# Performance work log

Measured on AMD Instinct MI355X. Metric: run time of the kernel, lower is better.

Reference implementation:

```python
import jax, jax.numpy as jnp
import numpy as np

TOP_K = 2  # k experts per token


def setup_inputs() -> dict:
    key = jax.random.key(0)
    ks = jax.random.split(key, 6)
    B, L, D, E, F = 2, 2048, 1024, 8, 4096
    x = jax.random.normal(ks[0], (B, L, D), dtype=jnp.float32)
    Wg = jax.random.normal(ks[1], (D, E), dtype=jnp.float32) * (D ** -0.5)
    W1 = jax.random.normal(ks[2], (E, D, F), dtype=jnp.float32) * (D ** -0.5)
    b1 = jnp.zeros((E, F), dtype=jnp.float32)
    W2 = jax.random.normal(ks[3], (E, F, D), dtype=jnp.float32) * (F ** -0.5)
    b2 = jnp.zeros((E, D), dtype=jnp.float32)
    return {"x": x, "Wg": Wg, "W1": W1, "b1": b1, "W2": W2, "b2": b2}


def reference(x, Wg, W1, b1, W2, b2):
    b, l, d = x.shape
    E = Wg.shape[1]
    xt = x.reshape(b * l, d)                      # (N, D)
    N = xt.shape[0]
    # Router: sigmoid gate, top-k (gate weights are NOT renormalized in the source)
    S = jax.nn.sigmoid(xt @ Wg)                   # (N, E)
    G, I = jax.lax.top_k(S, TOP_K)                # (N, k) each
    # Dense equivalent of per-expert gather-MLP-scatter: run every expert
    # on every token, then combine with the sparse top-k routing weights.
    h = jax.nn.gelu(jnp.einsum('nd,edf->enf', xt, W1) + b1[:, None, :])  # (E, N, F)
    y = jnp.einsum('enf,efd->end', h, W2) + b2[:, None, :]               # (E, N, D)
    # combine[n, e] = sum of gate values for slots routed to expert e
    combine = jnp.zeros((N, E), dtype=x.dtype).at[jnp.arange(N)[:, None], I].add(G)
    out = jnp.einsum('ne,end->nd', combine, y)    # (N, D)
    return out.reshape(b, l, d)
```

## Files before the change

### kernel.cpp

```cpp
#include <hip/hip_runtime.h>
#include <math.h>

typedef __bf16 bf16_t;
typedef __attribute__((ext_vector_type(8))) __bf16 bf16x8;
typedef __attribute__((ext_vector_type(4))) __bf16 bf16x4;
typedef __attribute__((ext_vector_type(4))) float f32x4;

#define NTOK 4096
#define DDIM 1024
#define FDIM 4096
#define NEXP 8
#define CAP  4096
#define HROWS (2*NTOK + 128)
#define NPAIR (2*NTOK)

#define GLOAD_LDS16(g, l) \
  __builtin_amdgcn_global_load_lds((__attribute__((address_space(1))) void*)(g), \
                                   (__attribute__((address_space(3))) void*)(l), 16, 0, 0)

__device__ __forceinline__ float fast_gelu(float v) {
  float u = 0.7978845608028654f * (v + 0.044715f * v * v * v);
  float uc = fminf(fmaxf(u, -10.f), 10.f);
  float t = __builtin_amdgcn_exp2f(2.885390081777927f * uc);
  float th = (t - 1.f) * __builtin_amdgcn_rcpf(t + 1.f);
  return 0.5f * v * (1.0f + th);
}

__global__ __launch_bounds__(256) void init_kernel(const float4* __restrict__ x4,
                                                   bf16x4* __restrict__ xbf4,
                                                   int n4, int* __restrict__ cnts) {
  int i = blockIdx.x * 256 + threadIdx.x;
  if (i < n4) {
    float4 v = x4[i];
    bf16x4 o;
    o.x = (bf16_t)v.x; o.y = (bf16_t)v.y; o.z = (bf16_t)v.z; o.w = (bf16_t)v.w;
    xbf4[i] = o;
  }
  if (i < NEXP) cnts[i] = 0;
}

__global__ __launch_bounds__(256) void transpose_cvt(const float* __restrict__ in,
                                                     bf16_t* __restrict__ outp,
                                                     int R, int C) {
  __shared__ float tile[64][65];
  int e = blockIdx.z;
  const float* ip = in + (size_t)e * R * C;
  bf16_t* op = outp + (size_t)e * R * C;
  int c0 = blockIdx.x * 64, r0 = blockIdx.y * 64;
  int rr = threadIdx.x >> 4;
  int cc = (threadIdx.x & 15) * 4;
#pragma unroll
  for (int p = 0; p < 4; p++) {
    float4 v = *(const float4*)(ip + (size_t)(r0 + p * 16 + rr) * C + c0 + cc);
    tile[p * 16 + rr][cc + 0] = v.x;
    tile[p * 16 + rr][cc + 1] = v.y;
    tile[p * 16 + rr][cc + 2] = v.z;
    tile[p * 16 + rr][cc + 3] = v.w;
  }
  __syncthreads();
  int c = threadIdx.x >> 3;
  int r8 = (threadIdx.x & 7) * 8;
#pragma unroll
  for (int p = 0; p < 2; p++) {
    int cp = c + p * 32;
    bf16x8 o;
#pragma unroll
    for (int i = 0; i < 8; i++) o[i] = (bf16_t)tile[r8 + i][cp];
    *(bf16x8*)(op + (size_t)(c0 + cp) * R + r0 + r8) = o;
  }
}

__global__ __launch_bounds__(256) void router_kernel(const float* __restrict__ x,
                                                     const float* __restrict__ Wg,
                                                     int* __restrict__ tokL,
                                                     int* __restrict__ cnts,
                                                     int* __restrict__ pairE,
                                                     int* __restrict__ pairS,
                                                     float* __restrict__ pairG) {
  int wid = threadIdx.x >> 6, lane = threadIdx.x & 63;
  int n = blockIdx.x * 4 + wid;
  const float* xr = x + (size_t)n * DDIM;
  double acc[NEXP];
#pragma unroll
  for (int e = 0; e < NEXP; e++) acc[e] = 0.0;
  for (int i = 0; i < DDIM / 64; i++) {
    int d = i * 64 + lane;
    float xv = xr[d];
    const float* wr = Wg + (size_t)d * NEXP;
#pragma unroll
    for (int e = 0; e < NEXP; e++) acc[e] += (double)xv * (double)wr[e];
  }
#pragma unroll
  for (int e = 0; e < NEXP; e++) {
    double v = acc[e];
#pragma unroll
    for (int off = 32; off; off >>= 1) v += __shfl_xor(v, off);
    acc[e] = v;
  }
  if (lane == 0) {
    int i1 = -1, i2 = -1;
    double s1 = -1e300, s2 = -1e300;
#pragma unroll
    for (int e = 0; e < NEXP; e++) {
      double v = acc[e];
      if (v > s1) { s2 = s1; i2 = i1; s1 = v; i1 = e; }
      else if (v > s2) { s2 = v; i2 = e; }
    }
    float g1 = 1.0f / (1.0f + expf((float)(-s1)));
    float g2 = 1.0f / (1.0f + expf((float)(-s2)));
    int p1 = atomicAdd(&cnts[i1], 1);
    tokL[i1 * CAP + p1] = n;
    int p2 = atomicAdd(&cnts[i2], 1);
    tokL[i2 * CAP + p2] = n;
    pairE[2 * n] = i1; pairS[2 * n] = p1; pairG[2 * n] = g1;
    pairE[2 * n + 1] = i2; pairS[2 * n + 1] = p2; pairG[2 * n + 1] = g2;
  }
}

__global__ void offs_kernel(const int* __restrict__ cnts, int* __restrict__ offs) {
  if (threadIdx.x == 0) {
    int s = 0;
    for (int e = 0; e < NEXP; e++) { offs[e] = s; s += cnts[e]; }
    offs[NEXP] = s;
  }
}

__global__ __launch_bounds__(256) void gemm1_kernel(
    const bf16_t* __restrict__ xbf, const bf16_t* __restrict__ wt1,
    const float* __restrict__ b1, const int* __restrict__ tokL,
    const int* __restrict__ cnts, const int* __restrict__ offs,
    bf16_t* __restrict__ H) {
  const int e = blockIdx.z;
  const int cnt = cnts[e];
  const int m0 = blockIdx.y * 128;
  if (m0 >= cnt) return;
  const int n0 = blockIdx.x * 128;
  const int t = threadIdx.x;

  __shared__ alignas(16) bf16_t As[128 * 32];
  __shared__ alignas(16) bf16_t Bs[128 * 32];

  const int sr = t >> 2;
  const int sc = (t & 3) * 8;
  const int r0 = m0 + sr, r1 = m0 + sr + 64;
  const int tok0 = (r0 < cnt) ? tokL[e * CAP + r0] : 0;
  const int tok1 = (r1 < cnt) ? tokL[e * CAP + r1] : 0;
  const bf16_t* gA0 = xbf + (size_t)tok0 * DDIM + sc;
  const bf16_t* gA1 = xbf + (size_t)tok1 * DDIM + sc;
  const bf16_t* wte = wt1 + (size_t)e * FDIM * DDIM;
  const bf16_t* gB0 = wte + (size_t)(n0 + sr) * DDIM + sc;
  const bf16_t* gB1 = wte + (size_t)(n0 + sr + 64) * DDIM + sc;
  bf16_t* lA0 = As + t * 8; bf16_t* lA1 = As + 2048 + t * 8;
  bf16_t* lB0 = Bs + t * 8; bf16_t* lB1 = Bs + 2048 + t * 8;

  const int lane = t & 63, w = t >> 6;
  const int wm = (w >> 1) * 64, wn = (w & 1) * 64;
  const int lid = lane & 15, quad = lane >> 4;

  f32x4 acc[4][4] = {};
  for (int kk = 0; kk < DDIM; kk += 32) {
    GLOAD_LDS16(gA0 + kk, lA0);
    GLOAD_LDS16(gA1 + kk, lA1);
    GLOAD_LDS16(gB0 + kk, lB0);
    GLOAD_LDS16(gB1 + kk, lB1);
    __syncthreads();
    bf16x8 af[4], bfm[4];
#pragma unroll
    for (int i = 0; i < 4; i++)
      af[i] = *(const bf16x8*)(As + (wm + i * 16 + lid) * 32 + quad * 8);
#pragma unroll
    for (int j = 0; j < 4; j++)
      bfm[j] = *(const bf16x8*)(Bs + (wn + j * 16 + lid) * 32 + quad * 8);
#pragma unroll
    for (int i = 0; i < 4; i++)
#pragma unroll
      for (int j = 0; j < 4; j++)
        acc[i][j] = __builtin_amdgcn_mfma_f32_16x16x32_bf16(af[i], bfm[j], acc[i][j], 0, 0, 0);
    __syncthreads();
  }

  const float* b1e = b1 + (size_t)e * FDIM;
  const int offe = offs[e];
#pragma unroll
  for (int i = 0; i < 4; i++) {
#pragma unroll
    for (int reg = 0; reg < 4; reg++) {
      int pos = m0 + wm + i * 16 + quad * 4 + reg;
      if (pos >= cnt) continue;
      size_t hrow = (size_t)(offe + pos);
#pragma unroll
      for (int j = 0; j < 4; j++) {
        int col = n0 + wn + j * 16 + lid;
        float v = acc[i][j][reg] + b1e[col];
        H[hrow * FDIM + col] = (bf16_t)fast_gelu(v);
      }
    }
  }
}

__global__ __launch_bounds__(256) void gemm2_kernel(
    const bf16_t* __restrict__ H, const bf16_t* __restrict__ wt2,
    const int* __restrict__ cnts, const int* __restrict__ offs,
    float* __restrict__ Y0, float* __restrict__ Y1) {
  const int e = blockIdx.z;
  const int cnt = cnts[e];
  const int by = blockIdx.y;
  const int m0 = (by >> 1) * 128;
  const int split = by & 1;
  if (m0 >= cnt) return;
  const int n0 = blockIdx.x * 128;
  const int t = threadIdx.x;
  const int offe = offs[e];
  const int k0 = split * (FDIM / 2);

  __shared__ alignas(16) bf16_t As[128 * 32];
  __shared__ alignas(16) bf16_t Bs[128 * 32];

  const int sr = t >> 2;
  const int sc = (t & 3) * 8;
  const bf16_t* gA0 = H + (size_t)(offe + m0 + sr) * FDIM + sc + k0;
  const bf16_t* gA1 = H + (size_t)(offe + m0 + sr + 64) * FDIM + sc + k0;
  const bf16_t* wte = wt2 + (size_t)e * DDIM * FDIM;
  const bf16_t* gB0 = wte + (size_t)(n0 + sr) * FDIM + sc + k0;
  const bf16_t* gB1 = wte + (size_t)(n0 + sr + 64) * FDIM + sc + k0;
  bf16_t* lA0 = As + t * 8; bf16_t* lA1 = As + 2048 + t * 8;
  bf16_t* lB0 = Bs + t * 8; bf16_t* lB1 = Bs + 2048 + t * 8;

  const int lane = t & 63, w = t >> 6;
  const int wm = (w >> 1) * 64, wn = (w & 1) * 64;
  const int lid = lane & 15, quad = lane >> 4;

  f32x4 acc[4][4] = {};
  for (int kk = 0; kk < FDIM / 2; kk += 32) {
    GLOAD_LDS16(gA0 + kk, lA0);
    GLOAD_LDS16(gA1 + kk, lA1);
    GLOAD_LDS16(gB0 + kk, lB0);
    GLOAD_LDS16(gB1 + kk, lB1);
    __syncthreads();
    bf16x8 af[4], bfm[4];
#pragma unroll
    for (int i = 0; i < 4; i++)
      af[i] = *(const bf16x8*)(As + (wm + i * 16 + lid) * 32 + quad * 8);
#pragma unroll
    for (int j = 0; j < 4; j++)
      bfm[j] = *(const bf16x8*)(Bs + (wn + j * 16 + lid) * 32 + quad * 8);
#pragma unroll
    for (int i = 0; i < 4; i++)
#pragma unroll
      for (int j = 0; j < 4; j++)
        acc[i][j] = __builtin_amdgcn_mfma_f32_16x16x32_bf16(af[i], bfm[j], acc[i][j], 0, 0, 0);
    __syncthreads();
  }

  float* Ye = split ? Y1 : Y0;
#pragma unroll
  for (int i = 0; i < 4; i++) {
#pragma unroll
    for (int reg = 0; reg < 4; reg++) {
      int pos = m0 + wm + i * 16 + quad * 4 + reg;
      if (pos >= cnt) continue;
      float* yrow = Ye + (size_t)(offe + pos) * DDIM;
#pragma unroll
      for (int j = 0; j < 4; j++) {
        int col = n0 + wn + j * 16 + lid;
        yrow[col] = acc[i][j][reg];
      }
    }
  }
}

__global__ __launch_bounds__(256) void combine_kernel(
    const float* __restrict__ Y0, const float* __restrict__ Y1,
    const float* __restrict__ b2, const int* __restrict__ pairE,
    const int* __restrict__ pairS, const float* __restrict__ pairG,
    const int* __restrict__ offs, float4* __restrict__ out4) {
  const int n = blockIdx.x;
  const int e1 = pairE[2 * n], e2 = pairE[2 * n + 1];
  const int r1 = offs[e1] + pairS[2 * n];
  const int r2 = offs[e2] + pairS[2 * n + 1];
  const float g1 = pairG[2 * n], g2 = pairG[2 * n + 1];
  const int t = threadIdx.x;
  const float4* ya0 = (const float4*)(Y0 + (size_t)r1 * DDIM);
  const float4* ya1 = (const float4*)(Y1 + (size_t)r1 * DDIM);
  const float4* yb0 = (const float4*)(Y0 + (size_t)r2 * DDIM);
  const float4* yb1 = (const float4*)(Y1 + (size_t)r2 * DDIM);
  const float4* ba = (const float4*)(b2 + (size_t)e1 * DDIM);
  const float4* bb = (const float4*)(b2 + (size_t)e2 * DDIM);
  float4 a0 = ya0[t], a1 = ya1[t], c0 = yb0[t], c1 = yb1[t];
  float4 pa = ba[t], pb = bb[t];
  float4 o;
  o.x = g1 * (a0.x + a1.x + pa.x) + g2 * (c0.x + c1.x + pb.x);
  o.y = g1 * (a0.y + a1.y + pa.y) + g2 * (c0.y + c1.y + pb.y);
  o.z = g1 * (a0.z + a1.z + pa.z) + g2 * (c0.z + c1.z + pb.z);
  o.w = g1 * (a0.w + a1.w + pa.w) + g2 * (c0.w + c1.w + pb.w);
  out4[(size_t)n * (DDIM / 4) + t] = o;
}

extern "C" void kernel_launch(void* const* d_in, const int* in_sizes, int n_in,
                              void* d_out, int out_size, void* d_ws, size_t ws_size,
                              hipStream_t stream) {
  const float* x  = (const float*)d_in[0];
  const float* Wg = (const float*)d_in[1];
  const float* W1 = (const float*)d_in[2];
  const float* b1 = (const float*)d_in[3];
  const float* W2 = (const float*)d_in[4];
  const float* b2 = (const float*)d_in[5];
  float* out = (float*)d_out;

  char* ws = (char*)d_ws;
  size_t off = 0;
  auto alloc = [&](size_t bytes) -> void* {
    void* p = (void*)(ws + off);
    off += (bytes + 255) & ~(size_t)255;
    return p;
  };
  bf16_t* xbf   = (bf16_t*)alloc((size_t)NTOK * DDIM * 2);
  bf16_t* wt1   = (bf16_t*)alloc((size_t)NEXP * FDIM * DDIM * 2);
  bf16_t* wt2   = (bf16_t*)alloc((size_t)NEXP * DDIM * FDIM * 2);
  bf16_t* H     = (bf16_t*)alloc((size_t)HROWS * FDIM * 2);
  int*    tokL  = (int*)alloc((size_t)NEXP * CAP * 4);
  int*    pairE = (int*)alloc((size_t)NPAIR * 4);
  int*    pairS = (int*)alloc((size_t)NPAIR * 4);
  float*  pairG = (float*)alloc((size_t)NPAIR * 4);
  int*    cnts  = (int*)alloc(64);
  int*    offs  = (int*)alloc(64);
  if (off > ws_size) return;

  float* Y0 = (float*)wt1;
  float* Y1 = Y0 + (size_t)NPAIR * DDIM / 2 * 2;
  Y1 = Y0 + (size_t)8192 * DDIM;

  const int n4 = NTOK * DDIM / 4;
  init_kernel<<<(n4 + 255) / 256, 256, 0, stream>>>((const float4*)x, (bf16x4*)xbf,
                                                    n4, cnts);
  transpose_cvt<<<dim3(FDIM / 64, DDIM / 64, NEXP), 256, 0, stream>>>(W1, wt1, DDIM, FDIM);
  transpose_cvt<<<dim3(DDIM / 64, FDIM / 64, NEXP), 256, 0, stream>>>(W2, wt2, FDIM, DDIM);
  router_kernel<<<NTOK / 4, 256, 0, stream>>>(x, Wg, tokL, cnts, pairE, pairS, pairG);
  offs_kernel<<<1, 64, 0, stream>>>(cnts, offs);
  gemm1_kernel<<<dim3(FDIM / 128, CAP / 128, NEXP), 256, 0, stream>>>(
      xbf, wt1, b1, tokL, cnts, offs, H);
  gemm2_kernel<<<dim3(DDIM / 128, (CAP / 128) * 2, NEXP), 256, 0, stream>>>(
      H, wt2, cnts, offs, Y0, Y1);
  combine_kernel<<<NTOK, 256, 0, stream>>>(Y0, Y1, b2, pairE, pairS, pairG, offs,
                                           (float4*)out);
}
```

Before: 703.5 us.

## Fuse prep kernels and launch compact per-expert block list for GEMMs

Merges the input conversion, both weight transposes and the router into a single prep kernel with larger 128x64 transpose tiles, and replaces the count-reset init with a memset. offs_kernel now builds a compact list of (expert, row-start) blocks so the GEMMs launch only up to 72 row blocks instead of 32 per expert, most of which exited early. This cuts launch count and the cost of scheduling empty blocks. The risk is that the 64x129 float LDS tile lowers occupancy for the transpose branch, and that MAXB=72 must cover every block the routing can produce.

```diff
diff --git a/kernel.cpp b/kernel.cpp
--- a/kernel.cpp
+++ b/kernel.cpp
@@ -13,6 +13,7 @@
 #define CAP  4096
 #define HROWS (2*NTOK + 128)
 #define NPAIR (2*NTOK)
+#define MAXB 72
 
 #define GLOAD_LDS16(g, l) \
   __builtin_amdgcn_global_load_lds((__attribute__((address_space(1))) void*)(g), \
@@ -26,102 +27,115 @@
   return 0.5f * v * (1.0f + th);
 }
 
-__global__ __launch_bounds__(256) void init_kernel(const float4* __restrict__ x4,
-                                                   bf16x4* __restrict__ xbf4,
-                                                   int n4, int* __restrict__ cnts) {
-  int i = blockIdx.x * 256 + threadIdx.x;
-  if (i < n4) {
-    float4 v = x4[i];
+__device__ __forceinline__ void tile_transpose(const float* __restrict__ ip,
+                                               bf16_t* __restrict__ op,
+                                               int R, int C, int r0, int c0,
+                                               float* tileT, int t) {
+#pragma unroll
+  for (int it = 0; it < 8; it++) {
+    int idx = it * 256 + t;
+    int row = idx >> 4;
+    int c4 = (idx & 15) << 2;
+    float4 v = *(const float4*)(ip + (size_t)(r0 + row) * C + c0 + c4);
+    tileT[(c4 + 0) * 129 + row] = v.x;
+    tileT[(c4 + 1) * 129 + row] = v.y;
+    tileT[(c4 + 2) * 129 + row] = v.z;
+    tileT[(c4 + 3) * 129 + row] = v.w;
+  }
+  __syncthreads();
+  int c = t >> 2;
+  int rs = (t & 3) * 32;
+  const float* src = tileT + c * 129 + rs;
+  bf16_t* dst = op + (size_t)(c0 + c) * R + r0 + rs;
+#pragma unroll
+  for (int seg = 0; seg < 4; seg++) {
+    bf16x8 o;
+#pragma unroll
+    for (int i = 0; i < 8; i++) o[i] = (bf16_t)src[seg * 8 + i];
+    *(bf16x8*)(dst + seg * 8) = o;
+  }
+}
+
+__global__ __launch_bounds__(256) void prep_kernel(
+    const float* __restrict__ W1, const float* __restrict__ W2,
+    const float* __restrict__ x, const float* __restrict__ Wg,
+    bf16_t* __restrict__ wt1, bf16_t* __restrict__ wt2,
+    bf16_t* __restrict__ xbf, int* __restrict__ tokL, int* __restrict__ cnts,
+    int* __restrict__ pairE, int* __restrict__ pairS, float* __restrict__ pairG) {
+  __shared__ float tileT[64 * 129];
+  const int b = blockIdx.x;
+  const int t = threadIdx.x;
+  if (b < 4096) {
+    int e = b >> 9, ti = b & 511;
+    int r0 = (ti & 7) * 128, c0 = (ti >> 3) * 64;
+    tile_transpose(W1 + (size_t)e * DDIM * FDIM, wt1 + (size_t)e * DDIM * FDIM,
+                   DDIM, FDIM, r0, c0, tileT, t);
+  } else if (b < 8192) {
+    int b0 = b - 4096;
+    int e = b0 >> 9, ti = b0 & 511;
+    int r0 = (ti & 31) * 128, c0 = (ti >> 5) * 64;
+    tile_transpose(W2 + (size_t)e * FDIM * DDIM, wt2 + (size_t)e * FDIM * DDIM,
+                   FDIM, DDIM, r0, c0, tileT, t);
+  } else if (b < 12288) {
+    int i = (b - 8192) * 256 + t;
+    float4 v = ((const float4*)x)[i];
     bf16x4 o;
     o.x = (bf16_t)v.x; o.y = (bf16_t)v.y; o.z = (bf16_t)v.z; o.w = (bf16_t)v.w;
-    xbf4[i] = o;
-  }
-  if (i < NEXP) cnts[i] = 0;
-}
-
-__global__ __launch_bounds__(256) void transpose_cvt(const float* __restrict__ in,
-                                                     bf16_t* __restrict__ outp,
-                                                     int R, int C) {
-  __shared__ float tile[64][65];
-  int e = blockIdx.z;
-  const float* ip = in + (size_t)e * R * C;
-  bf16_t* op = outp + (size_t)e * R * C;
-  int c0 = blockIdx.x * 64, r0 = blockIdx.y * 64;
-  int rr = threadIdx.x >> 4;
-  int cc = (threadIdx.x & 15) * 4;
-#pragma unroll
-  for (int p = 0; p < 4; p++) {
-    float4 v = *(const float4*)(ip + (size_t)(r0 + p * 16 + rr) * C + c0 + cc);
-    tile[p * 16 + rr][cc + 0] = v.x;
-    tile[p * 16 + rr][cc + 1] = v.y;
-    tile[p * 16 + rr][cc + 2] = v.z;
-    tile[p * 16 + rr][cc + 3] = v.w;
-  }
-  __syncthreads();
-  int c = threadIdx.x >> 3;
-  int r8 = (threadIdx.x & 7) * 8;
-#pragma unroll
-  for (int p = 0; p < 2; p++) {
-    int cp = c + p * 32;
-    bf16x8 o;
-#pragma unroll
-    for (int i = 0; i < 8; i++) o[i] = (bf16_t)tile[r8 + i][cp];
-    *(bf16x8*)(op + (size_t)(c0 + cp) * R + r0 + r8) = o;
-  }
-}
-
-__global__ __launch_bounds__(256) void router_kernel(const float* __restrict__ x,
-                                                     const float* __restrict__ Wg,
-                                                     int* __restrict__ tokL,
-                                                     int* __restrict__ cnts,
-                                                     int* __restrict__ pairE,
-                                                     int* __restrict__ pairS,
-                                                     float* __restrict__ pairG) {
-  int wid = threadIdx.x >> 6, lane = threadIdx.x & 63;
-  int n = blockIdx.x * 4 + wid;
-  const float* xr = x + (size_t)n * DDIM;
-  double acc[NEXP];
-#pragma unroll
-  for (int e = 0; e < NEXP; e++) acc[e] = 0.0;
-  for (int i = 0; i < DDIM / 64; i++) {
-    int d = i * 64 + lane;
-    float xv = xr[d];
-    const float* wr = Wg + (size_t)d * NEXP;
-#pragma unroll
-    for (int e = 0; e < NEXP; e++) acc[e] += (double)xv * (double)wr[e];
-  }
-#pragma unroll
-  for (int e = 0; e < NEXP; e++) {
-    double v = acc[e];
-#pragma unroll
-    for (int off = 32; off; off >>= 1) v += __shfl_xor(v, off);
-    acc[e] = v;
-  }
-  if (lane == 0) {
-    int i1 = -1, i2 = -1;
-    double s1 = -1e300, s2 = -1e300;
+    ((bf16x4*)xbf)[i] = o;
+  } else {
+    int b0 = b - 12288;
+    int wid = t >> 6, lane = t & 63;
+    int n = b0 * 4 + wid;
+    const float* xr = x + (size_t)n * DDIM;
+    double acc[NEXP];
+#pragma unroll
+    for (int e = 0; e < NEXP; e++) acc[e] = 0.0;
+    for (int i = 0; i < DDIM / 64; i++) {
+      int d = i * 64 + lane;
+      float xv = xr[d];
+      const float* wr = Wg + (size_t)d * NEXP;
+#pragma unroll
+      for (int e = 0; e < NEXP; e++) acc[e] += (double)xv * (double)wr[e];
+    }
 #pragma unroll
     for (int e = 0; e < NEXP; e++) {
       double v = acc[e];
-      if (v > s1) { s2 = s1; i2 = i1; s1 = v; i1 = e; }
-      else if (v > s2) { s2 = v; i2 = e; }
-    }
-    float g1 = 1.0f / (1.0f + expf((float)(-s1)));
-    float g2 = 1.0f / (1.0f + expf((float)(-s2)));
-    int p1 = atomicAdd(&cnts[i1], 1);
-    tokL[i1 * CAP + p1] = n;
-    int p2 = atomicAdd(&cnts[i2], 1);
-    tokL[i2 * CAP + p2] = n;
-    pairE[2 * n] = i1; pairS[2 * n] = p1; pairG[2 * n] = g1;
-    pairE[2 * n + 1] = i2; pairS[2 * n + 1] = p2; pairG[2 * n + 1] = g2;
-  }
-}
-
-__global__ void offs_kernel(const int* __restrict__ cnts, int* __restrict__ offs) {
+#pragma unroll
+      for (int off = 32; off; off >>= 1) v += __shfl_xor(v, off);
+      acc[e] = v;
+    }
+    if (lane == 0) {
+      int i1 = -1, i2 = -1;
+      double s1 = -1e300, s2 = -1e300;
+#pragma unroll
+      for (int e = 0; e < NEXP; e++) {
+        double v = acc[e];
+        if (v > s1) { s2 = s1; i2 = i1; s1 = v; i1 = e; }
+        else if (v > s2) { s2 = v; i2 = e; }
+      }
+      float g1 = 1.0f / (1.0f + expf((float)(-s1)));
+      float g2 = 1.0f / (1.0f + expf((float)(-s2)));
+      int p1 = atomicAdd(&cnts[i1], 1);
+      tokL[i1 * CAP + p1] = n;
+      int p2 = atomicAdd(&cnts[i2], 1);
+      tokL[i2 * CAP + p2] = n;
+      pairE[2 * n] = i1; pairS[2 * n] = p1; pairG[2 * n] = g1;
+      pairE[2 * n + 1] = i2; pairS[2 * n + 1] = p2; pairG[2 * n + 1] = g2;
+    }
+  }
+}
+
+__global__ void offs_kernel(const int* __restrict__ cnts, int* __restrict__ offs,
+                            int* __restrict__ blkE, int* __restrict__ blkS) {
   if (threadIdx.x == 0) {
-    int s = 0;
-    for (int e = 0; e < NEXP; e++) { offs[e] = s; s += cnts[e]; }
+    int s = 0, nb = 0;
+    for (int e = 0; e < NEXP; e++) {
+      offs[e] = s;
+      for (int st = 0; st < cnts[e]; st += 128) { blkE[nb] = e; blkS[nb] = st; nb++; }
+      s += cnts[e];
+    }
     offs[NEXP] = s;
+    for (; nb < MAXB; nb++) { blkE[nb] = NEXP; blkS[nb] = 0; }
   }
 }
 
@@ -129,11 +143,12 @@
     const bf16_t* __restrict__ xbf, const bf16_t* __restrict__ wt1,
     const float* __restrict__ b1, const int* __restrict__ tokL,
     const int* __restrict__ cnts, const int* __restrict__ offs,
+    const int* __restrict__ blkE, const int* __restrict__ blkS,
     bf16_t* __restrict__ H) {
-  const int e = blockIdx.z;
+  const int e = blkE[blockIdx.y];
+  if (e >= NEXP) return;
+  const int m0 = blkS[blockIdx.y];
   const int cnt = cnts[e];
-  const int m0 = blockIdx.y * 128;
-  if (m0 >= cnt) return;
   const int n0 = blockIdx.x * 128;
   const int t = threadIdx.x;
 
@@ -201,13 +216,14 @@
 __global__ __launch_bounds__(256) void gemm2_kernel(
     const bf16_t* __restrict__ H, const bf16_t* __restrict__ wt2,
     const int* __restrict__ cnts, const int* __restrict__ offs,
+    const int* __restrict__ blkE, const int* __restrict__ blkS,
     float* __restrict__ Y0, float* __restrict__ Y1) {
-  const int e = blockIdx.z;
+  const int bi = blockIdx.y >> 1;
+  const int split = blockIdx.y & 1;
+  const int e = blkE[bi];
+  if (e >= NEXP) return;
+  const int m0 = blkS[bi];
   const int cnt = cnts[e];
-  const int by = blockIdx.y;
-  const int m0 = (by >> 1) * 128;
-  const int split = by & 1;
-  if (m0 >= cnt) return;
   const int n0 = blockIdx.x * 128;
   const int t = threadIdx.x;
   const int offe = offs[e];
@@ -324,23 +340,21 @@
   float*  pairG = (float*)alloc((size_t)NPAIR * 4);
   int*    cnts  = (int*)alloc(64);
   int*    offs  = (int*)alloc(64);
+  int*    blkE  = (int*)alloc(MAXB * 4);
+  int*    blkS  = (int*)alloc(MAXB * 4);
   if (off > ws_size) return;
 
   float* Y0 = (float*)wt1;
-  float* Y1 = Y0 + (size_t)NPAIR * DDIM / 2 * 2;
-  Y1 = Y0 + (size_t)8192 * DDIM;
-
-  const int n4 = NTOK * DDIM / 4;
-  init_kernel<<<(n4 + 255) / 256, 256, 0, stream>>>((const float4*)x, (bf16x4*)xbf,
-                                                    n4, cnts);
-  transpose_cvt<<<dim3(FDIM / 64, DDIM / 64, NEXP), 256, 0, stream>>>(W1, wt1, DDIM, FDIM);
-  transpose_cvt<<<dim3(DDIM / 64, FDIM / 64, NEXP), 256, 0, stream>>>(W2, wt2, FDIM, DDIM);
-  router_kernel<<<NTOK / 4, 256, 0, stream>>>(x, Wg, tokL, cnts, pairE, pairS, pairG);
-  offs_kernel<<<1, 64, 0, stream>>>(cnts, offs);
-  gemm1_kernel<<<dim3(FDIM / 128, CAP / 128, NEXP), 256, 0, stream>>>(
-      xbf, wt1, b1, tokL, cnts, offs, H);
-  gemm2_kernel<<<dim3(DDIM / 128, (CAP / 128) * 2, NEXP), 256, 0, stream>>>(
-      H, wt2, cnts, offs, Y0, Y1);
+  float* Y1 = Y0 + (size_t)8192 * DDIM;
+
+  hipMemsetAsync(cnts, 0, 64, stream);
+  prep_kernel<<<13312, 256, 0, stream>>>(W1, W2, x, Wg, wt1, wt2, xbf, tokL, cnts,
+                                         pairE, pairS, pairG);
+  offs_kernel<<<1, 64, 0, stream>>>(cnts, offs, blkE, blkS);
+  gemm1_kernel<<<dim3(FDIM / 128, MAXB), 256, 0, stream>>>(
+      xbf, wt1, b1, tokL, cnts, offs, blkE, blkS, H);
+  gemm2_kernel<<<dim3(DDIM / 128, MAXB * 2), 256, 0, stream>>>(
+      H, wt2, cnts, offs, blkE, blkS, Y0, Y1);
   combine_kernel<<<NTOK, 256, 0, stream>>>(Y0, Y1, b2, pairE, pairS, pairG, offs,
                                            (float4*)out);
 }
```

After: 697.2 us. About the same (-0.9%).
